# Optimization experiments

Measured on AMD Instinct MI355X. Metric: run time of the kernel, lower is better.

Reference implementation:

```python
import jax, jax.numpy as jnp
import numpy as np

INPUT_SIZE = 128
HIDDEN_SIZE = 1024
OUTPUT_SIZE = 64
E_PROP = 0.8
E_SIZE = int(E_PROP * HIDDEN_SIZE)  # 819
I_SIZE = HIDDEN_SIZE - E_SIZE       # 205


def _make_mask():
    # rows of [+1]*E_SIZE + [-1]*I_SIZE, zero diagonal (no self-connection)
    row = np.concatenate([np.ones(E_SIZE), -np.ones(I_SIZE)]).astype(np.float32)
    mask = np.tile(row, (HIDDEN_SIZE, 1))
    np.fill_diagonal(mask, 0.0)
    return jnp.asarray(mask)


def setup_inputs() -> dict:
    key = jax.random.key(0)
    ks = jax.random.split(key, 8)
    T, B = 512, 64
    scale = 1.0 / np.sqrt(HIDDEN_SIZE)
    x = jax.random.normal(ks[0], (T, B, INPUT_SIZE), dtype=jnp.float32)
    w_ih = jax.random.normal(ks[1], (HIDDEN_SIZE, INPUT_SIZE), dtype=jnp.float32) / np.sqrt(INPUT_SIZE)
    b_ih = jax.random.uniform(ks[2], (HIDDEN_SIZE,), minval=-scale, maxval=scale, dtype=jnp.float32)
    w_hh = jax.random.normal(ks[3], (HIDDEN_SIZE, HIDDEN_SIZE), dtype=jnp.float32) * scale
    # mimic reset_parameters: shrink excitatory columns by e_size/i_size ratio
    w_hh = w_hh.at[:, :E_SIZE].divide(E_SIZE / I_SIZE)
    b_hh = jax.random.uniform(ks[4], (HIDDEN_SIZE,), minval=-scale, maxval=scale, dtype=jnp.float32)
    w_fc = jax.random.normal(ks[5], (OUTPUT_SIZE, E_SIZE), dtype=jnp.float32) / np.sqrt(E_SIZE)
    b_fc = jax.random.uniform(ks[6], (OUTPUT_SIZE,), minval=-scale, maxval=scale, dtype=jnp.float32)
    # NOTE: RNN.__init__ hard-codes alpha = 1 regardless of the value passed in.
    alpha = jnp.array([1.0], dtype=jnp.float32)
    mask = _make_mask()
    return {"x": x, "w_ih": w_ih, "b_ih": b_ih, "w_hh": w_hh, "b_hh": b_hh,
            "w_fc": w_fc, "b_fc": b_fc, "alpha": alpha, "mask": mask}


def reference(x, w_ih, b_ih, w_hh, b_hh, w_fc, b_fc, alpha, mask):
    # x: (T, B, I). Precompute input projection for all timesteps (one big GEMM).
    inp_proj = jnp.einsum('tbi,hi->tbh', x, w_ih) + b_ih  # (T, B, H)
    # effective E-I weight: sign-constrained, zero diagonal; constant across steps
    eff_w = jnp.abs(w_hh) * mask                           # (H, H)
    a = alpha[0]
    B = x.shape[1]
    state0 = jnp.zeros((B, HIDDEN_SIZE), dtype=x.dtype)
    out0 = jnp.zeros((B, HIDDEN_SIZE), dtype=x.dtype)

    def step(carry, u_t):
        state, output = carry
        total = u_t + output @ eff_w.T + b_hh             # (B, H)
        state = a * (total - state) + state               # alpha blend (sigma_rec = 0)
        output = jnp.tanh(state)
        return (state, output), output

    _, rnn_activity = jax.lax.scan(step, (state0, out0), inp_proj)  # (T, B, H)
    rnn_e = rnn_activity[:, :, :E_SIZE]                   # excitatory readout only
    out = jnp.einsum('tbe,oe->tbo', rnn_e, w_fc) + b_fc   # (T, B, O)
    return out, rnn_activity
```

## Files before the change

### kernel.cpp

```cpp
#include <hip/hip_runtime.h>
#include <cmath>

#define T_STEPS 512
#define BATCH   64
#define HID     1024
#define INSZ    128
#define ESZ     819
#define OSZ     64

#define WS_EFFW   0
#define WS_WIHT   1048576
#define WS_HIST   1179648
#define WS_BADJ   34734080
#define WS_WFCP   34742272

typedef float f32x4 __attribute__((ext_vector_type(4)));

__global__ void prep_effw(const float* __restrict__ w_hh, const float* __restrict__ mask,
                          float* __restrict__ eff) {
    const int i = (blockIdx.x * 256 + threadIdx.x) * 4;
    const float4 w = *(const float4*)(w_hh + i);
    const float4 m = *(const float4*)(mask + i);
    float4 r;
    r.x = fabsf(w.x) * m.x; r.y = fabsf(w.y) * m.y;
    r.z = fabsf(w.z) * m.z; r.w = fabsf(w.w) * m.w;
    *(float4*)(eff + i) = r;
}

__global__ void prep_wihT(const float* __restrict__ w_ih, float* __restrict__ w_ihT) {
    const int idx = blockIdx.x * 256 + threadIdx.x;
    const int i = idx >> 10, h = idx & 1023;
    w_ihT[idx] = w_ih[h * INSZ + i];
}

__global__ void prep_wfc(const float* __restrict__ w_fc, const float* __restrict__ b_fc,
                         float* __restrict__ w_fcp, float* __restrict__ badj) {
    __shared__ float red[256];
    const int o = blockIdx.x, tid = threadIdx.x;
    float s = 0.f;
    for (int e = tid; e < 820; e += 256) {
        const float w = (e < ESZ) ? w_fc[o * ESZ + e] : 0.f;
        w_fcp[o * 820 + e] = w;
        s += w;
    }
    red[tid] = s;
    __syncthreads();
    for (int st = 128; st; st >>= 1) {
        if (tid < st) red[tid] += red[tid + st];
        __syncthreads();
    }
    if (tid == 0) badj[o] = b_fc[o] - 2.0f * red[0];
}

__global__ void inp_proj(const float* __restrict__ x, const float* __restrict__ w_ihT,
                         const float* __restrict__ b_ih, float* __restrict__ u) {
    __shared__ float xs[INSZ * 64];
    const int t = blockIdx.x, tid = threadIdx.x;
    const float* xt = x + (size_t)t * BATCH * INSZ;
    for (int k = tid * 4; k < BATCH * INSZ; k += 1024) {
        const float4 v = *(const float4*)(xt + k);
        const int b = k >> 7, i = k & 127;
        xs[(i + 0) * 64 + b] = v.x; xs[(i + 1) * 64 + b] = v.y;
        xs[(i + 2) * 64 + b] = v.z; xs[(i + 3) * 64 + b] = v.w;
    }
    __syncthreads();
    for (int hp = 0; hp < 2; ++hp) {
        const int h = hp * 512 + tid * 2;
        const float bi0 = b_ih[h], bi1 = b_ih[h + 1];
        for (int b0 = 0; b0 < 64; b0 += 8) {
            float acc0[8], acc1[8];
#pragma unroll
            for (int bb = 0; bb < 8; ++bb) { acc0[bb] = 0.f; acc1[bb] = 0.f; }
#pragma unroll 4
            for (int i = 0; i < INSZ; ++i) {
                const float2 w2 = *(const float2*)(w_ihT + i * 1024 + h);
                const float4 xa = *(const float4*)(xs + i * 64 + b0);
                const float4 xb = *(const float4*)(xs + i * 64 + b0 + 4);
                const float xv[8] = {xa.x, xa.y, xa.z, xa.w, xb.x, xb.y, xb.z, xb.w};
#pragma unroll
                for (int bb = 0; bb < 8; ++bb) {
                    acc0[bb] = fmaf(w2.x, xv[bb], acc0[bb]);
                    acc1[bb] = fmaf(w2.y, xv[bb], acc1[bb]);
                }
            }
#pragma unroll
            for (int bb = 0; bb < 8; ++bb) {
                float2 r; r.x = acc0[bb] + bi0; r.y = acc1[bb] + bi1;
                *(float2*)(u + ((size_t)(b0 + bb) * T_STEPS + t) * 1024 + h) = r;
            }
        }
    }
}

#define ISSUE2(VA, VB, SRC)                                               \
    asm volatile("global_load_dwordx4 %0, %2, off sc0\n\t"                \
                 "global_load_dwordx4 %1, %2, off offset:512 sc0"         \
                 : "=&v"(VA), "=&v"(VB) : "v"(SRC) : "memory")
#define WAIT2(VA, VB)                                                     \
    asm volatile("s_waitcnt vmcnt(0)" : "+v"(VA), "+v"(VB) :: "memory")
#define RELOAD2(VA, VB, SRC)                                              \
    asm volatile("global_load_dwordx4 %0, %2, off sc0 sc1\n\t"            \
                 "global_load_dwordx4 %1, %2, off offset:512 sc0 sc1\n\t" \
                 "s_waitcnt vmcnt(0)"                                     \
                 : "=&v"(VA), "=&v"(VB) : "v"(SRC) : "memory")

__device__ __forceinline__ float min8f(f32x4 x, f32x4 y) {
    return fminf(fminf(fminf(x[0], x[1]), fminf(x[2], x[3])),
                 fminf(fminf(y[0], y[1]), fminf(y[2], y[3])));
}

__global__ void __launch_bounds__(256, 1)
rnn_scan(const float* __restrict__ eff_w, const float* __restrict__ u,
         const float* __restrict__ b_hh, const float* __restrict__ alpha,
         float* __restrict__ hist) {
    extern __shared__ float smem[];
    float* w_s = smem;
    float* pp  = smem + 32768;
    const int tid = threadIdx.x, wg = blockIdx.x;
    const int bg = wg & 7, hgrp = wg >> 3;
    const int h0 = hgrp << 5, b0 = bg << 3;

    float rsum = 0.f;
    {
        const int hl = tid >> 3, grp = hl >> 2, l4 = hl & 3;
        const int j0 = (tid & 7) << 7;
        const float* wrow = eff_w + (size_t)(h0 + hl) * 1024;
        for (int j = j0; j < j0 + 128; j += 4) {
            const float4 w4 = *(const float4*)(wrow + j);
            w_s[((j + 0) << 5) + (((grp + j + 0) & 7) << 2) + l4] = w4.x;
            w_s[((j + 1) << 5) + (((grp + j + 1) & 7) << 2) + l4] = w4.y;
            w_s[((j + 2) << 5) + (((grp + j + 2) & 7) << 2) + l4] = w4.z;
            w_s[((j + 3) << 5) + (((grp + j + 3) & 7) << 2) + l4] = w4.w;
            rsum += (w4.x + w4.y) + (w4.z + w4.w);
        }
    }
    rsum += __shfl_xor(rsum, 1);
    rsum += __shfl_xor(rsum, 2);
    rsum += __shfl_xor(rsum, 4);

    const float a = alpha[0];
    const int r_hl = tid >> 3, r_b = tid & 7;
    const int rh = h0 + r_hl, rb = b0 + r_b;
    const float bias0 = b_hh[rh];
    const float bias_eff = bias0 - 2.0f * rsum;
    const size_t u_base = ((size_t)rb * T_STEPS) * 1024 + rh;
    float* const my_hist = hist + ((size_t)rb * T_STEPS) * 1024 + rh;
    const int hp = tid >> 5, jc = tid & 31;
    const int b_s = tid >> 5, q = tid & 31;
    const float* const sbase = hist + ((size_t)(b0 + b_s) * T_STEPS) * 1024 + (q << 2);
    const int s1 = ((q & 7) + (q >> 3)) & 7;
    const int s2 = (s1 + 4) & 7;
    const int ppA = (b_s << 10) + ((q >> 3) << 5) + (s1 << 2);
    const int ppB = (b_s << 10) + 128 + ((q >> 3) << 5) + (s2 << 2);
    const int cbase = ((hgrp >> 3) + 1) & 3;
    float state = 0.f;
    f32x4 vA, vB;
    __syncthreads();

    for (int t = 0; t < T_STEPS; ++t) {
        const float uval = u[u_base + ((size_t)t << 10)];
        float red = 0.f;
        if (t > 0) {
            const float* srow = sbase + ((size_t)(t - 1) << 10);
            float acc[4][8];
#pragma unroll
            for (int i = 0; i < 4; ++i)
#pragma unroll
                for (int b = 0; b < 8; ++b) acc[i][b] = 0.f;

            int cc = cbase;
            for (int k = 0; k < 4; ++k) {
                {
                    const float* sc = srow + (cc << 8);
                    WAIT2(vA, vB);
                    float mn = min8f(vA, vB);
                    while (!(mn >= 1.0f)) {
                        __builtin_amdgcn_s_sleep(1);
                        RELOAD2(vA, vB, sc);
                        mn = min8f(vA, vB);
                    }
                    *(f32x4*)(pp + (cc << 8) + ppA) = vA;
                    *(f32x4*)(pp + (cc << 8) + ppB) = vB;
                }
                __syncthreads();
                if (k < 3) { const float* nsrc = srow + ((((cc + 1) & 3)) << 8); ISSUE2(vA, vB, nsrc); }
#pragma unroll
                for (int l = 0; l < 8; ++l) {
                    const int jjg = (cc << 3) + l;
                    const int j = (jjg << 5) + jc;
                    const f32x4 wv = *(const f32x4*)&w_s[(j << 5) + (((hp + j) & 7) << 2)];
                    const int phij = (jjg << 5) + ((((jc >> 2) + jjg) & 7) << 2) + (jc & 3);
                    float pv[8];
#pragma unroll
                    for (int b = 0; b < 8; ++b) pv[b] = pp[(b << 10) + phij];
#pragma unroll
                    for (int b = 0; b < 8; ++b) {
                        acc[0][b] = fmaf(wv[0], pv[b], acc[0][b]);
                        acc[1][b] = fmaf(wv[1], pv[b], acc[1][b]);
                        acc[2][b] = fmaf(wv[2], pv[b], acc[2][b]);
                        acc[3][b] = fmaf(wv[3], pv[b], acc[3][b]);
                    }
                }
                cc = (cc + 1) & 3;
            }
            __syncthreads();
#pragma unroll
            for (int i = 0; i < 4; ++i)
#pragma unroll
                for (int b = 0; b < 8; ++b) {
                    const int oo = ((hp << 2) + i) * 8 + b;
                    pp[(oo << 5) + ((jc + oo) & 31)] = acc[i][b];
                }
            __syncthreads();
#pragma unroll
            for (int k = 0; k < 32; ++k)
                red += pp[(tid << 5) + ((k + tid) & 31)];
        }
        const float tot = uval + red + ((t > 0) ? bias_eff : bias0);
        state = fmaf(a, tot - state, state);
        const float ov = tanhf(state);
        __hip_atomic_store(my_hist + ((size_t)t << 10), ov + 2.0f, __ATOMIC_RELAXED,
                           __HIP_MEMORY_SCOPE_AGENT);
        { const float* nsrc = sbase + ((size_t)t << 10) + (cbase << 8); ISSUE2(vA, vB, nsrc); }
        __syncthreads();
    }
}

__global__ void copy_act(const float* __restrict__ hist, float* __restrict__ act) {
    const int t = blockIdx.x >> 6, b = blockIdx.x & 63;
    const float* src = hist + ((size_t)b * T_STEPS + t) * 1024 + threadIdx.x * 4;
    float* dst = act + ((size_t)t * BATCH + b) * 1024 + threadIdx.x * 4;
    float4 v = *(const float4*)src;
    v.x -= 2.0f; v.y -= 2.0f; v.z -= 2.0f; v.w -= 2.0f;
    *(float4*)dst = v;
}

__global__ void fc_out(const float* __restrict__ hist, const float* __restrict__ w_fcp,
                       const float* __restrict__ badj, float* __restrict__ out0) {
    __shared__ float hs[16 * 820];
    const int t = blockIdx.x >> 2, bq = blockIdx.x & 3, tid = threadIdx.x;
    const int b0 = bq << 4;
    for (int r = 0; r < 16; ++r) {
        const float* src = hist + ((size_t)(b0 + r) * T_STEPS + t) * 1024;
        for (int e = tid; e < 820; e += 256) hs[r * 820 + e] = (e < ESZ) ? src[e] : 0.f;
    }
    __syncthreads();
    const int bb = tid >> 4, ol = tid & 15;
    float acc[4] = {0.f, 0.f, 0.f, 0.f};
    const float* hrow = hs + bb * 820;
    for (int e = 0; e < 820; e += 4) {
        const float4 hv = *(const float4*)(hrow + e);
#pragma unroll
        for (int k = 0; k < 4; ++k) {
            const float4 wv = *(const float4*)(w_fcp + (size_t)(ol + (k << 4)) * 820 + e);
            acc[k] += hv.x * wv.x + hv.y * wv.y + hv.z * wv.z + hv.w * wv.w;
        }
    }
    const int b = b0 + bb;
#pragma unroll
    for (int k = 0; k < 4; ++k) {
        const int o = ol + (k << 4);
        out0[((size_t)t * BATCH + b) * OSZ + o] = acc[k] + badj[o];
    }
}

extern "C" void kernel_launch(void* const* d_in, const int* in_sizes, int n_in,
                              void* d_out, int out_size, void* d_ws, size_t ws_size,
                              hipStream_t stream) {
    const float* x     = (const float*)d_in[0];
    const float* w_ih  = (const float*)d_in[1];
    const float* b_ih  = (const float*)d_in[2];
    const float* w_hh  = (const float*)d_in[3];
    const float* b_hh  = (const float*)d_in[4];
    const float* w_fc  = (const float*)d_in[5];
    const float* b_fc  = (const float*)d_in[6];
    const float* alpha = (const float*)d_in[7];
    const float* mask  = (const float*)d_in[8];

    float* out  = (float*)d_out;
    float* out0 = out;
    float* act  = out + (size_t)T_STEPS * BATCH * OSZ;

    float* ws     = (float*)d_ws;
    float* eff_w  = ws + WS_EFFW;
    float* w_ihT  = ws + WS_WIHT;
    float* hist   = ws + WS_HIST;
    float* badj   = ws + WS_BADJ;
    float* w_fcp  = ws + WS_WFCP;
    float* u      = act;

    hipMemsetAsync(hist, 0, (size_t)BATCH * T_STEPS * HID * sizeof(float), stream);
    prep_effw<<<1024, 256, 0, stream>>>(w_hh, mask, eff_w);
    prep_wihT<<<512, 256, 0, stream>>>(w_ih, w_ihT);
    prep_wfc<<<64, 256, 0, stream>>>(w_fc, b_fc, w_fcp, badj);
    inp_proj<<<512, 256, 0, stream>>>(x, w_ihT, b_ih, u);

    hipFuncSetAttribute(reinterpret_cast<const void*>(rnn_scan),
                        hipFuncAttributeMaxDynamicSharedMemorySize, 163840);
    void* args[] = {(void*)&eff_w, (void*)&u, (void*)&b_hh, (void*)&alpha, (void*)&hist};
    hipLaunchCooperativeKernel(reinterpret_cast<const void*>(rnn_scan),
                               dim3(256), dim3(256), args, 163840, stream);

    copy_act<<<32768, 256, 0, stream>>>(hist, act);
    fc_out<<<2048, 256, 0, stream>>>(hist, w_fcp, badj, out0);
}
```

Before: 4.177 ms.

## Map batch groups to XCDs dynamically and poll L2 before bypassing cache

Each workgroup reads its XCD id and claims a slot through an atomic counter, so all workgroups that share a batch group sit on the same XCD and exchange hidden state through that XCD's L2. If the distribution is not exactly 32 per XCD, it falls back to the static mapping. Polling first uses L2-scoped reloads and only bypasses the cache after 16 tries. A second plain store is added alongside the atomic store so the value lands in the local L2. The cost is an extra grid sync at startup plus the extra store, and correctness now depends on cache coherence behaviour across XCDs.

```diff
diff --git a/kernel.cpp b/kernel.cpp
--- a/kernel.cpp
+++ b/kernel.cpp
@@ -1,4 +1,5 @@
 #include <hip/hip_runtime.h>
+#include <hip/hip_cooperative_groups.h>
 #include <cmath>
 
 #define T_STEPS 512
@@ -12,6 +13,7 @@
 #define WS_WIHT   1048576
 #define WS_HIST   1179648
 #define WS_BADJ   34734080
+#define WS_CNT    34734144
 #define WS_WFCP   34742272
 
 typedef float f32x4 __attribute__((ext_vector_type(4)));
@@ -98,7 +100,12 @@
                  : "=&v"(VA), "=&v"(VB) : "v"(SRC) : "memory")
 #define WAIT2(VA, VB)                                                     \
     asm volatile("s_waitcnt vmcnt(0)" : "+v"(VA), "+v"(VB) :: "memory")
-#define RELOAD2(VA, VB, SRC)                                              \
+#define RELOAD2_L2(VA, VB, SRC)                                           \
+    asm volatile("global_load_dwordx4 %0, %2, off sc0\n\t"                \
+                 "global_load_dwordx4 %1, %2, off offset:512 sc0\n\t"     \
+                 "s_waitcnt vmcnt(0)"                                     \
+                 : "=&v"(VA), "=&v"(VB) : "v"(SRC) : "memory")
+#define RELOAD2_IC(VA, VB, SRC)                                           \
     asm volatile("global_load_dwordx4 %0, %2, off sc0 sc1\n\t"            \
                  "global_load_dwordx4 %1, %2, off offset:512 sc0 sc1\n\t" \
                  "s_waitcnt vmcnt(0)"                                     \
@@ -112,13 +119,34 @@
 __global__ void __launch_bounds__(256, 1)
 rnn_scan(const float* __restrict__ eff_w, const float* __restrict__ u,
          const float* __restrict__ b_hh, const float* __restrict__ alpha,
-         float* __restrict__ hist) {
+         float* __restrict__ hist, unsigned* __restrict__ cnt) {
     extern __shared__ float smem[];
     float* w_s = smem;
     float* pp  = smem + 32768;
     const int tid = threadIdx.x, wg = blockIdx.x;
-    const int bg = wg & 7, hgrp = wg >> 3;
+
+    if (tid == 0) {
+        unsigned xcd;
+        asm volatile("s_getreg_b32 %0, hwreg(HW_REG_XCC_ID)" : "=s"(xcd));
+        xcd &= 7;
+        const unsigned slot = atomicAdd(cnt + xcd, 1u);
+        ((unsigned*)pp)[0] = xcd;
+        ((unsigned*)pp)[1] = slot;
+    }
+    cooperative_groups::this_grid().sync();
+    if (tid == 0) {
+        unsigned ok = 1;
+        for (int x = 0; x < 8; ++x)
+            ok &= (__hip_atomic_load(cnt + x, __ATOMIC_RELAXED,
+                                     __HIP_MEMORY_SCOPE_AGENT) == 32u) ? 1u : 0u;
+        ((unsigned*)pp)[2] = ok;
+    }
+    __syncthreads();
+    const unsigned dynok = ((unsigned*)pp)[2];
+    const int bg   = dynok ? (int)((unsigned*)pp)[0]        : (wg & 7);
+    const int hgrp = dynok ? (int)(((unsigned*)pp)[1] & 31) : (wg >> 3);
     const int h0 = hgrp << 5, b0 = bg << 3;
+    __syncthreads();
 
     float rsum = 0.f;
     {
@@ -174,9 +202,11 @@
                     const float* sc = srow + (cc << 8);
                     WAIT2(vA, vB);
                     float mn = min8f(vA, vB);
+                    int tries = 0;
                     while (!(mn >= 1.0f)) {
                         __builtin_amdgcn_s_sleep(1);
-                        RELOAD2(vA, vB, sc);
+                        if (tries < 16) { RELOAD2_L2(vA, vB, sc); ++tries; }
+                        else            { RELOAD2_IC(vA, vB, sc); }
                         mn = min8f(vA, vB);
                     }
                     *(f32x4*)(pp + (cc << 8) + ppA) = vA;
@@ -219,8 +249,10 @@
         const float tot = uval + red + ((t > 0) ? bias_eff : bias0);
         state = fmaf(a, tot - state, state);
         const float ov = tanhf(state);
-        __hip_atomic_store(my_hist + ((size_t)t << 10), ov + 2.0f, __ATOMIC_RELAXED,
-                           __HIP_MEMORY_SCOPE_AGENT);
+        const float tagged = ov + 2.0f;
+        float* pst = my_hist + ((size_t)t << 10);
+        __hip_atomic_store(pst, tagged, __ATOMIC_RELAXED, __HIP_MEMORY_SCOPE_AGENT);
+        asm volatile("global_store_dword %0, %1, off" :: "v"(pst), "v"(tagged) : "memory");
         { const float* nsrc = sbase + ((size_t)t << 10) + (cbase << 8); ISSUE2(vA, vB, nsrc); }
         __syncthreads();
     }
@@ -286,10 +318,12 @@
     float* w_ihT  = ws + WS_WIHT;
     float* hist   = ws + WS_HIST;
     float* badj   = ws + WS_BADJ;
+    unsigned* cnt = (unsigned*)(ws + WS_CNT);
     float* w_fcp  = ws + WS_WFCP;
     float* u      = act;
 
     hipMemsetAsync(hist, 0, (size_t)BATCH * T_STEPS * HID * sizeof(float), stream);
+    hipMemsetAsync(cnt, 0, 8 * sizeof(unsigned), stream);
     prep_effw<<<1024, 256, 0, stream>>>(w_hh, mask, eff_w);
     prep_wihT<<<512, 256, 0, stream>>>(w_ih, w_ihT);
     prep_wfc<<<64, 256, 0, stream>>>(w_fc, b_fc, w_fcp, badj);
@@ -297,7 +331,8 @@
 
     hipFuncSetAttribute(reinterpret_cast<const void*>(rnn_scan),
                         hipFuncAttributeMaxDynamicSharedMemorySize, 163840);
-    void* args[] = {(void*)&eff_w, (void*)&u, (void*)&b_hh, (void*)&alpha, (void*)&hist};
+    void* args[] = {(void*)&eff_w, (void*)&u, (void*)&b_hh, (void*)&alpha,
+                    (void*)&hist, (void*)&cnt};
     hipLaunchCooperativeKernel(reinterpret_cast<const void*>(rnn_scan),
                                dim3(256), dim3(256), args, 163840, stream);
 
```

New measurement: 5.954 ms. +42.6%, slower.

## Replace LDS transpose reduction with wave shuffles and lighter barriers in RNN scan

Applied to the files above, without the earlier changes.

The per-step cross-lane reduction of the 32 partial accumulators moves from an LDS write, a barrier and a strided read to a recursive-halving butterfly of __shfl_xor operations within each 32-lane group. Each lane ends up with the same output index as before. This removes two workgroup barriers and the LDS round trip from the serial recurrence. The remaining __syncthreads calls become a bare s_barrier preceded only by an lgkmcnt wait, so in-flight prefetch global loads are no longer drained at each barrier. The cost is extra shuffle and select instructions and more reliance on hand-written wait counts.

```diff
diff --git a/kernel.cpp b/kernel.cpp
--- a/kernel.cpp
+++ b/kernel.cpp
@@ -103,6 +103,10 @@
                  "global_load_dwordx4 %1, %2, off offset:512 sc0 sc1\n\t" \
                  "s_waitcnt vmcnt(0)"                                     \
                  : "=&v"(VA), "=&v"(VB) : "v"(SRC) : "memory")
+
+#define RAWBAR()                                                          \
+    do { asm volatile("s_waitcnt lgkmcnt(0)" ::: "memory");               \
+         __builtin_amdgcn_s_barrier(); } while (0)
 
 __device__ __forceinline__ float min8f(f32x4 x, f32x4 y) {
     return fminf(fminf(fminf(x[0], x[1]), fminf(x[2], x[3])),
@@ -162,11 +166,9 @@
         float red = 0.f;
         if (t > 0) {
             const float* srow = sbase + ((size_t)(t - 1) << 10);
-            float acc[4][8];
-#pragma unroll
-            for (int i = 0; i < 4; ++i)
-#pragma unroll
-                for (int b = 0; b < 8; ++b) acc[i][b] = 0.f;
+            float A[32];
+#pragma unroll
+            for (int i = 0; i < 32; ++i) A[i] = 0.f;
 
             int cc = cbase;
             for (int k = 0; k < 4; ++k) {
@@ -182,7 +184,7 @@
                     *(f32x4*)(pp + (cc << 8) + ppA) = vA;
                     *(f32x4*)(pp + (cc << 8) + ppB) = vB;
                 }
-                __syncthreads();
+                RAWBAR();
                 if (k < 3) { const float* nsrc = srow + ((((cc + 1) & 3)) << 8); ISSUE2(vA, vB, nsrc); }
 #pragma unroll
                 for (int l = 0; l < 8; ++l) {
@@ -195,26 +197,44 @@
                     for (int b = 0; b < 8; ++b) pv[b] = pp[(b << 10) + phij];
 #pragma unroll
                     for (int b = 0; b < 8; ++b) {
-                        acc[0][b] = fmaf(wv[0], pv[b], acc[0][b]);
-                        acc[1][b] = fmaf(wv[1], pv[b], acc[1][b]);
-                        acc[2][b] = fmaf(wv[2], pv[b], acc[2][b]);
-                        acc[3][b] = fmaf(wv[3], pv[b], acc[3][b]);
+                        A[0 * 8 + b] = fmaf(wv[0], pv[b], A[0 * 8 + b]);
+                        A[1 * 8 + b] = fmaf(wv[1], pv[b], A[1 * 8 + b]);
+                        A[2 * 8 + b] = fmaf(wv[2], pv[b], A[2 * 8 + b]);
+                        A[3 * 8 + b] = fmaf(wv[3], pv[b], A[3 * 8 + b]);
                     }
                 }
                 cc = (cc + 1) & 3;
             }
-            __syncthreads();
-#pragma unroll
-            for (int i = 0; i < 4; ++i)
-#pragma unroll
-                for (int b = 0; b < 8; ++b) {
-                    const int oo = ((hp << 2) + i) * 8 + b;
-                    pp[(oo << 5) + ((jc + oo) & 31)] = acc[i][b];
-                }
-            __syncthreads();
-#pragma unroll
-            for (int k = 0; k < 32; ++k)
-                red += pp[(tid << 5) + ((k + tid) & 31)];
+#pragma unroll
+            for (int r = 0; r < 16; ++r) {
+                const float give = (tid & 16) ? A[r] : A[r + 16];
+                const float keep = (tid & 16) ? A[r + 16] : A[r];
+                A[r] = keep + __shfl_xor(give, 16, 64);
+            }
+#pragma unroll
+            for (int r = 0; r < 8; ++r) {
+                const float give = (tid & 8) ? A[r] : A[r + 8];
+                const float keep = (tid & 8) ? A[r + 8] : A[r];
+                A[r] = keep + __shfl_xor(give, 8, 64);
+            }
+#pragma unroll
+            for (int r = 0; r < 4; ++r) {
+                const float give = (tid & 4) ? A[r] : A[r + 4];
+                const float keep = (tid & 4) ? A[r + 4] : A[r];
+                A[r] = keep + __shfl_xor(give, 4, 64);
+            }
+#pragma unroll
+            for (int r = 0; r < 2; ++r) {
+                const float give = (tid & 2) ? A[r] : A[r + 2];
+                const float keep = (tid & 2) ? A[r + 2] : A[r];
+                A[r] = keep + __shfl_xor(give, 2, 64);
+            }
+            {
+                const float give = (tid & 1) ? A[0] : A[1];
+                const float keep = (tid & 1) ? A[1] : A[0];
+                A[0] = keep + __shfl_xor(give, 1, 64);
+            }
+            red = A[0];
         }
         const float tot = uval + red + ((t > 0) ? bias_eff : bias0);
         state = fmaf(a, tot - state, state);
@@ -222,7 +242,7 @@
         __hip_atomic_store(my_hist + ((size_t)t << 10), ov + 2.0f, __ATOMIC_RELAXED,
                            __HIP_MEMORY_SCOPE_AGENT);
         { const float* nsrc = sbase + ((size_t)t << 10) + (cbase << 8); ISSUE2(vA, vB, nsrc); }
-        __syncthreads();
+        RAWBAR();
     }
 }
 
```

Measured after the change: 4.062 ms. 2.7% less time.
